# Kernel optimization log

Measured on AMD Instinct MI355X. Metric: run time of the kernel, lower is better.

## Reference

```python
import jax, jax.numpy as jnp
import numpy as np

EPS = 1e-5

def conv(x, w, groups=1):
    # x: NCHW, w: OIHW, VALID padding, stride 1 (cross-correlation, same as torch conv2d)
    return jax.lax.conv_general_dilated(x, w, (1, 1), 'VALID',
                                        feature_group_count=groups,
                                        dimension_numbers=('NCHW', 'OIHW', 'NCHW'))

def bn(x, g, b, m, v):
    # eval-mode batchnorm with running stats
    scale = (g / jnp.sqrt(v + EPS))[None, :, None, None]
    return (x - m[None, :, None, None]) * scale + b[None, :, None, None]

def xcorr_depthwise(x, k):
    # x: [B,C,Hs,Ws] search, k: [B,C,Hk,Wk] per-sample kernels
    B, C, H, W = x.shape
    xr = x.reshape(1, B * C, H, W)
    kr = k.reshape(B * C, 1, k.shape[2], k.shape[3])
    out = conv(xr, kr, groups=B * C)  # [1, B*C, Ho, Wo]
    return out.reshape(B, C, out.shape[2], out.shape[3])

def setup_inputs() -> dict:
    key = jax.random.key(0)
    ks = jax.random.split(key, 16)
    Cin, Hid, Cout = 256, 256, 20
    inp = {
        'kernel': jax.random.normal(ks[0], (128, Cin, 7, 7), jnp.float32),
        'search': jax.random.normal(ks[1], (128, Cin, 31, 31), jnp.float32),
        'wk': jax.random.normal(ks[2], (Hid, Cin, 3, 3), jnp.float32) * 0.02,
        'gk': jnp.ones((Hid,), jnp.float32),
        'bk': jnp.zeros((Hid,), jnp.float32),
        'mk': jax.random.normal(ks[3], (Hid,), jnp.float32) * 0.1,
        'vk': jax.random.uniform(ks[4], (Hid,), jnp.float32) + 0.5,
        'ws': jax.random.normal(ks[5], (Hid, Cin, 3, 3), jnp.float32) * 0.02,
        'gs': jnp.ones((Hid,), jnp.float32),
        'bs': jnp.zeros((Hid,), jnp.float32),
        'ms': jax.random.normal(ks[6], (Hid,), jnp.float32) * 0.1,
        'vs': jax.random.uniform(ks[7], (Hid,), jnp.float32) + 0.5,
        'wh1': jax.random.normal(ks[8], (Hid, Hid, 1, 1), jnp.float32) * 0.02,
        'gh': jnp.ones((Hid,), jnp.float32),
        'bh': jnp.zeros((Hid,), jnp.float32),
        'mh': jax.random.normal(ks[9], (Hid,), jnp.float32) * 0.1,
        'vh': jax.random.uniform(ks[10], (Hid,), jnp.float32) + 0.5,
        'wh2': jax.random.normal(ks[11], (Cout, Hid, 1, 1), jnp.float32) * 0.02,
        'bh2': jnp.zeros((Cout,), jnp.float32),
    }
    return inp

def reference(kernel, search, wk, gk, bk, mk, vk, ws, gs, bs, ms, vs,
              wh1, gh, bh, mh, vh, wh2, bh2):
    k = jax.nn.relu(bn(conv(kernel, wk), gk, bk, mk, vk))   # [B,256,5,5]
    s = jax.nn.relu(bn(conv(search, ws), gs, bs, ms, vs))   # [B,256,29,29]
    f = xcorr_depthwise(s, k)                               # [B,256,25,25]
    h = jax.nn.relu(bn(conv(f, wh1), gh, bh, mh, vh))
    out = conv(h, wh2) + bh2[None, :, None, None]           # [B,20,25,25]
    return out
```

## Files before the change

### kernel.cpp

```cpp
#include <hip/hip_runtime.h>

typedef __bf16 bf16x8 __attribute__((ext_vector_type(8)));
typedef float floatx4 __attribute__((ext_vector_type(4)));
typedef unsigned short u16;
typedef unsigned int u32;

__device__ __forceinline__ u16 f2bf(float f) {
    union { float f; unsigned int u; } q; q.f = f;
    unsigned int r = q.u + 0x7FFFu + ((q.u >> 16) & 1u);
    return (u16)(r >> 16);
}
__device__ __forceinline__ float bf2f(u16 b) {
    union { unsigned int u; float f; } q; q.u = ((unsigned int)b) << 16;
    return q.f;
}

__device__ __forceinline__ void gl2lds16(const u16* g, u16* l) {
    __builtin_amdgcn_global_load_lds((const __attribute__((address_space(1))) u32*)g,
                                     (__attribute__((address_space(3))) u32*)l, 16, 0, 0);
}

__global__ __launch_bounds__(256) void prep_all(
    const float* __restrict__ wk, const float* __restrict__ wsw, const float* __restrict__ wh1,
    const float* __restrict__ gk, const float* __restrict__ bk,
    const float* __restrict__ mk, const float* __restrict__ vk,
    const float* __restrict__ gs, const float* __restrict__ bs,
    const float* __restrict__ ms, const float* __restrict__ vs,
    const float* __restrict__ gh, const float* __restrict__ bh,
    const float* __restrict__ mh, const float* __restrict__ vh,
    u16* __restrict__ WKP, u16* __restrict__ WSP, u16* __restrict__ WH1P,
    float* __restrict__ par)
{
    int bid = blockIdx.x, t = threadIdx.x;
    if (bid < 4608) {
        const float* src = (bid < 2304) ? wk : wsw;
        u16* dst = (bid < 2304) ? WKP : WSP;
        int tid = ((bid < 2304) ? bid : bid - 2304) * 256 + t;
        int o  = tid / 2304;
        int k  = tid - o * 2304;
        int rc = k >> 8;
        int ci = k & 255;
        dst[tid] = f2bf(src[o * 2304 + ci * 9 + rc]);
    } else if (bid < 4864) {
        int tid = (bid - 4608) * 256 + t;
        WH1P[tid] = f2bf(wh1[tid]);
    } else {
        float s;
        s = gk[t] * rsqrtf(vk[t] + 1e-5f); par[0*256+t] = s; par[1*256+t] = bk[t] - mk[t]*s;
        s = gs[t] * rsqrtf(vs[t] + 1e-5f); par[2*256+t] = s; par[3*256+t] = bs[t] - ms[t]*s;
        s = gh[t] * rsqrtf(vh[t] + 1e-5f); par[4*256+t] = s; par[5*256+t] = bh[t] - mh[t]*s;
    }
}

__global__ __launch_bounds__(256) void nchw2nhwc_both(
    const float* __restrict__ kin, u16* __restrict__ KIN,
    const float* __restrict__ sin_, u16* __restrict__ SIN)
{
    __shared__ float tile[64][33];
    int bid = blockIdx.x;
    const float* in; u16* out; int HW, sptiles;
    if (bid < 1024) { in = kin;  out = KIN; HW = 49;  sptiles = 2; }
    else { bid -= 1024; in = sin_; out = SIN; HW = 961; sptiles = 31; }
    int st  = bid % sptiles;
    int tmp = bid / sptiles;
    int ct  = tmp & 3;
    int b   = tmp >> 2;
    int sp0 = st * 32, ci0 = ct * 64;
    int t = threadIdx.x;
    int j = t & 31, i8 = t >> 5;
    const float* ip = in + ((size_t)b * 256 + ci0 + i8) * HW + sp0 + j;
#pragma unroll
    for (int k = 0; k < 8; ++k) {
        if (sp0 + j < HW) tile[i8 + k * 8][j] = ip[(size_t)(k * 8) * HW];
    }
    __syncthreads();
    int cl = t & 63, s4 = t >> 6;
#pragma unroll
    for (int k = 0; k < 8; ++k) {
        int spl = s4 + k * 4;
        int sp  = sp0 + spl;
        if (sp < HW) out[((size_t)b * HW + sp) * 256 + ci0 + cl] = f2bf(tile[cl][spl]);
    }
}

__global__ __launch_bounds__(256) void conv_gemm(
    const u16* __restrict__ Ain, const u16* __restrict__ Wpk,
    const float* __restrict__ scale, const float* __restrict__ shift,
    u16* __restrict__ Out,
    int OHW, int OW, int IW, int bstride, int KW, int nrc, int mblocks)
{
    __shared__ u16 Alds[4096];
    __shared__ u16 Blds[4096];

    const int tot = mblocks * 2;
    const int grp = (tot >> 3) << 3;
    const int lid = blockIdx.x;
    const int nid = (lid < grp) ? ((lid & 7) * (grp >> 3) + (lid >> 3)) : lid;
    const int m0 = (nid >> 1) * 128;
    const int n0 = (nid & 1) * 128;

    const int t    = threadIdx.x;
    const int wave = t >> 6;
    const int lane = t & 63;
    const int quad = lane >> 4;
    const int lrow = lane & 15;

    const int koff = (((t & 3) ^ ((t >> 3) & 3)) << 3);
    const int r0 = t >> 2;
    int m_a0 = m0 + r0;
    int b0 = m_a0 / OHW; int rem0 = m_a0 - b0 * OHW; int y0 = rem0 / OW; int x0 = rem0 - y0 * OW;
    int m_a1 = m_a0 + 64;
    int b1 = m_a1 / OHW; int rem1 = m_a1 - b1 * OHW; int y1 = rem1 / OW; int x1 = rem1 - y1 * OW;
    const u16* ag0 = Ain + (size_t)b0 * bstride + (size_t)(y0 * IW + x0) * 256 + koff;
    const u16* ag1 = Ain + (size_t)b1 * bstride + (size_t)(y1 * IW + x1) * 256 + koff;
    const int Ktot = nrc * 256;
    const u16* bg0 = Wpk + (size_t)(n0 + r0) * Ktot + koff;
    const u16* bg1 = bg0 + (size_t)64 * Ktot;

    u16* lA0 = Alds + wave * 512;
    u16* lA1 = Alds + 2048 + wave * 512;
    u16* lB0 = Blds + wave * 512;
    u16* lB1 = Blds + 2048 + wave * 512;

    floatx4 zero = {0.f, 0.f, 0.f, 0.f};
    floatx4 acc[4][4];
#pragma unroll
    for (int i = 0; i < 4; ++i)
#pragma unroll
        for (int j = 0; j < 4; ++j) acc[i][j] = zero;

    const int wr  = (wave >> 1) << 6;
    const int wc  = (wave & 1) << 6;
    const int pos = ((quad ^ ((lrow >> 1) & 3)) << 3);

    const int nchunks = nrc << 3;
    for (int ch = 0; ch < nchunks; ++ch) {
        int rc  = ch >> 3;
        int ci0 = (ch & 7) << 5;
        int rr  = rc / KW;
        int cc  = rc - rr * KW;
        int ao  = (rr * IW + cc) * 256 + ci0;
        int bo  = ch << 5;
        __syncthreads();
        gl2lds16(ag0 + ao, lA0);
        gl2lds16(ag1 + ao, lA1);
        gl2lds16(bg0 + bo, lB0);
        gl2lds16(bg1 + bo, lB1);
        __syncthreads();
        bf16x8 af[4], bfr[4];
#pragma unroll
        for (int mi = 0; mi < 4; ++mi)
            af[mi] = *(const bf16x8*)&Alds[(wr + mi * 16 + lrow) * 32 + pos];
#pragma unroll
        for (int ni = 0; ni < 4; ++ni)
            bfr[ni] = *(const bf16x8*)&Blds[(wc + ni * 16 + lrow) * 32 + pos];
#pragma unroll
        for (int mi = 0; mi < 4; ++mi)
#pragma unroll
            for (int ni = 0; ni < 4; ++ni)
                acc[mi][ni] = __builtin_amdgcn_mfma_f32_16x16x32_bf16(af[mi], bfr[ni], acc[mi][ni], 0, 0, 0);
    }

    float sc[4], sh[4];
#pragma unroll
    for (int ni = 0; ni < 4; ++ni) {
        int gn = n0 + wc + ni * 16 + lrow;
        sc[ni] = scale[gn];
        sh[ni] = shift[gn];
    }
#pragma unroll
    for (int mi = 0; mi < 4; ++mi) {
        int gm = m0 + wr + mi * 16 + (quad << 2);
#pragma unroll
        for (int ri = 0; ri < 4; ++ri) {
            size_t ro = (size_t)(gm + ri) * 256 + n0 + wc + lrow;
#pragma unroll
            for (int ni = 0; ni < 4; ++ni) {
                float v = acc[mi][ni][ri] * sc[ni] + sh[ni];
                v = fmaxf(v, 0.f);
                Out[ro + ni * 16] = f2bf(v);
            }
        }
    }
}

#define NS_BLK 421
__global__ __launch_bounds__(512, 2) void conv_gemm256(
    const u16* __restrict__ AinS, const u16* __restrict__ WpkS,
    const float* __restrict__ parS, u16* __restrict__ OutS,
    const u16* __restrict__ AinK, const u16* __restrict__ WpkK,
    const float* __restrict__ parK, u16* __restrict__ OutK)
{
    __shared__ __align__(16) u16 Alds[2][256][64];
    __shared__ __align__(16) u16 Blds[2][256][64];

    const int Ktot = 2304;
    const int NKT  = 36;
    const int KW   = 3;

    const int lid = blockIdx.x;
    const bool isk = (lid >= NS_BLK);

    int nid;
    if (!isk) {
        const int xcd = lid & 7, sub = lid >> 3;
        nid = (xcd < 5) ? (xcd * 53 + sub) : (265 + (xcd - 5) * 52 + sub);
    } else {
        nid = lid - NS_BLK;
    }
    const int m0 = nid << 8;

    const int OHW     = isk ? 25    : 841;
    const int OW      = isk ? 5     : 29;
    const int IW      = isk ? 7     : 31;
    const int bstride = isk ? 12544 : 246016;
    const int Mtot    = isk ? 3200  : 107648;
    const u16* Ain    = isk ? AinK : AinS;
    const u16* Wpk    = isk ? WpkK : WpkS;
    const float* scale = isk ? parK : parS;
    const float* shift = scale + 256;
    u16* Out          = isk ? OutK : OutS;

    const int t     = threadIdx.x;
    const int wave  = t >> 6;
    const int lane  = t & 63;
    const int lrow  = lane & 15;
    const int lquad = lane >> 4;
    const int wmBase = (wave >> 2) << 7;
    const int wnBase = (wave & 3) << 6;

    const u16* pA[4];
    const u16* pB[4];
#pragma unroll
    for (int j = 0; j < 4; ++j) {
        int u = j * 512 + t;
        int row = u >> 3, slot = u & 7;
        int ko = ((slot ^ (row & 7)) << 3);
        int m = m0 + row; if (m >= Mtot) m = Mtot - 1;
        int b = m / OHW; int rem = m - b * OHW; int y = rem / OW; int x = rem - y * OW;
        pA[j] = Ain + (size_t)b * bstride + (size_t)(y * IW + x) * 256 + ko;
        pB[j] = Wpk + (size_t)row * (size_t)Ktot + ko;
    }

    const int xo0 = ((lquad ^ (lrow & 7)) << 3);
    const int xo1 = xo0 ^ 32;

    floatx4 acc[8][4];
#pragma unroll
    for (int i = 0; i < 8; ++i)
#pragma unroll
        for (int j = 0; j < 4; ++j) acc[i][j] = (floatx4){0.f, 0.f, 0.f, 0.f};

#pragma unroll
    for (int j = 0; j < 4; ++j)
        gl2lds16(pA[j], &Alds[0][0][0] + j * 4096 + wave * 512);
#pragma unroll
    for (int j = 0; j < 4; ++j)
        gl2lds16(pB[j], &Blds[0][0][0] + j * 4096 + wave * 512);
    asm volatile("s_waitcnt vmcnt(0)" ::: "memory");
    __builtin_amdgcn_s_barrier();

#define LOADA(mb) do {                                              \
        const u16* _p = Ab + (wmBase + (mb) * 16 + lrow) * 64;      \
        aF[0][0] = *(const bf16x8*)(_p + xo0);                      \
        aF[0][1] = *(const bf16x8*)(_p + xo1);                      \
        aF[1][0] = *(const bf16x8*)(_p + 1024 + xo0);               \
        aF[1][1] = *(const bf16x8*)(_p + 1024 + xo1);               \
    } while (0)

#define MFMA16(mb) do {                                                                               \
        _Pragma("unroll")                                                                             \
        for (int _n = 0; _n < 4; ++_n) {                                                              \
            acc[(mb)][_n]     = __builtin_amdgcn_mfma_f32_16x16x32_bf16(aF[0][0], bB[_n][0], acc[(mb)][_n], 0, 0, 0);     \
            acc[(mb)][_n]     = __builtin_amdgcn_mfma_f32_16x16x32_bf16(aF[0][1], bB[_n][1], acc[(mb)][_n], 0, 0, 0);     \
            acc[(mb) + 1][_n] = __builtin_amdgcn_mfma_f32_16x16x32_bf16(aF[1][0], bB[_n][0], acc[(mb) + 1][_n], 0, 0, 0); \
            acc[(mb) + 1][_n] = __builtin_amdgcn_mfma_f32_16x16x32_bf16(aF[1][1], bB[_n][1], acc[(mb) + 1][_n], 0, 0, 0); \
        }                                                                                             \
    } while (0)

#define PH_MID() do {                                        \
        __builtin_amdgcn_s_barrier();                        \
        asm volatile("s_waitcnt lgkmcnt(0)" ::: "memory");   \
        __builtin_amdgcn_s_setprio(1);                       \
    } while (0)

#define PH_END() do {                                        \
        __builtin_amdgcn_s_setprio(0);                       \
        __builtin_amdgcn_s_barrier();                        \
    } while (0)

#pragma unroll 2
    for (int kt = 0; kt < NKT; ++kt) {
        const int c = kt & 1;
        const u16* Ab = &Alds[c][0][0];
        const u16* Bb = &Blds[c][0][0];
        u16* An = &Alds[c ^ 1][0][0];
        u16* Bn = &Blds[c ^ 1][0][0];
        const int pf = (kt + 1 < NKT);
        const int kt1 = kt + 1;
        const int rc = kt1 >> 2;
        const int rr = rc / KW;
        const int cc = rc - rr * KW;
        const int aoffA = (rr * IW + cc) * 256 + ((kt1 & 3) << 6);
        const int boffB = kt1 << 6;

        bf16x8 bB[4][2];
        bf16x8 aF[2][2];

#pragma unroll
        for (int ni = 0; ni < 4; ++ni) {
            const u16* _p = Bb + (wnBase + ni * 16 + lrow) * 64;
            bB[ni][0] = *(const bf16x8*)(_p + xo0);
            bB[ni][1] = *(const bf16x8*)(_p + xo1);
        }
        LOADA(0);
        if (pf) {
#pragma unroll
            for (int j = 0; j < 4; ++j)
                gl2lds16(pA[j] + aoffA, An + j * 4096 + wave * 512);
        }
        PH_MID();
        MFMA16(0);
        PH_END();

        LOADA(2);
        if (pf) {
#pragma unroll
            for (int j = 0; j < 4; ++j)
                gl2lds16(pB[j] + boffB, Bn + j * 4096 + wave * 512);
        }
        PH_MID();
        MFMA16(2);
        PH_END();

        LOADA(4);
        PH_MID();
        MFMA16(4);
        PH_END();

        LOADA(6);
        PH_MID();
        MFMA16(6);
        __builtin_amdgcn_s_setprio(0);
        asm volatile("s_waitcnt vmcnt(0)" ::: "memory");
        __builtin_amdgcn_s_barrier();
    }

#undef LOADA
#undef MFMA16
#undef PH_MID
#undef PH_END

    float sc[4], sh[4];
#pragma unroll
    for (int ni = 0; ni < 4; ++ni) {
        int gn = wnBase + ni * 16 + lrow;
        sc[ni] = scale[gn];
        sh[ni] = shift[gn];
    }
#pragma unroll
    for (int mi = 0; mi < 8; ++mi) {
        int gm0 = m0 + wmBase + mi * 16 + (lquad << 2);
#pragma unroll
        for (int ri = 0; ri < 4; ++ri) {
            int gm = gm0 + ri;
            if (gm < Mtot) {
                size_t ro = (size_t)gm * 256 + wnBase + lrow;
#pragma unroll
                for (int ni = 0; ni < 4; ++ni) {
                    float v = acc[mi][ni][ri] * sc[ni] + sh[ni];
                    v = fmaxf(v, 0.f);
                    Out[ro + ni * 16] = f2bf(v);
                }
            }
        }
    }
}

__global__ __launch_bounds__(256) void xcorr(const u16* __restrict__ ss, const u16* __restrict__ kk,
                                             u16* __restrict__ f) {
    int lid = blockIdx.x;
    int bid = (lid & 7) * 400 + (lid >> 3);
    int b = bid / 25, y = bid - b * 25;
    int t = threadIdx.x;
    int cg = (t & 31) << 3;
    int xg = t >> 5;
    const u16* kbase = kk + (size_t)b * 25 * 256 + cg;
    const u16* sbase = ss + (size_t)(b * 29 + y) * 29 * 256 + cg;

    float acc[4][8];
#pragma unroll
    for (int j = 0; j < 4; ++j)
#pragma unroll
        for (int e = 0; e < 8; ++e) acc[j][e] = 0.f;

#pragma unroll
    for (int r = 0; r < 5; ++r) {
        const u16* srow = sbase + (size_t)r * 29 * 256;
#pragma unroll
        for (int c = 0; c < 5; ++c) {
            bf16x8 kv = *(const bf16x8*)(kbase + (r * 5 + c) * 256);
            float kf[8];
#pragma unroll
            for (int e = 0; e < 8; ++e) kf[e] = (float)kv[e];
#pragma unroll
            for (int j = 0; j < 4; ++j) {
                int x = xg + 8 * j;
                if (x < 25) {
                    bf16x8 sv = *(const bf16x8*)(srow + (size_t)(x + c) * 256);
#pragma unroll
                    for (int e = 0; e < 8; ++e) acc[j][e] += (float)sv[e] * kf[e];
                }
            }
        }
    }

    u16* fb = f + (size_t)(b * 25 + y) * 25 * 256 + cg;
#pragma unroll
    for (int j = 0; j < 4; ++j) {
        int x = xg + 8 * j;
        if (x < 25) {
            u16 pk[8];
#pragma unroll
            for (int e = 0; e < 8; ++e) pk[e] = f2bf(acc[j][e]);
            *(bf16x8*)(fb + (size_t)x * 256) = *(const bf16x8*)pk;
        }
    }
}

__global__ __launch_bounds__(256) void head(const u16* __restrict__ h, const float* __restrict__ w2,
                                            const float* __restrict__ b2, float* __restrict__ out) {
    __shared__ __align__(16) u16   hl[25 * 264];
    __shared__ __align__(16) float wl[20 * 260];
    int bid = blockIdx.x;
    int b = bid / 25, y = bid - b * 25;
    int t = threadIdx.x;
    const u16* hrow = h + (size_t)(b * 25 + y) * 25 * 256;
    for (int i = t; i < 800; i += 256) {
        int x = i >> 5, c8 = i & 31;
        *(bf16x8*)&hl[x * 264 + c8 * 8] = *(const bf16x8*)&hrow[i * 8];
    }
    for (int i = t; i < 1280; i += 256) {
        int co = i >> 6, c4 = i & 63;
        *(float4*)&wl[co * 260 + c4 * 4] = *(const float4*)&w2[(size_t)co * 256 + c4 * 4];
    }
    __syncthreads();
    for (int o = t; o < 500; o += 256) {
        int x = o / 20, co = o - x * 20;
        float acc = b2[co];
        const u16* hp = &hl[x * 264];
        const float* wp = &wl[co * 260];
#pragma unroll 4
        for (int k = 0; k < 256; k += 8) {
            bf16x8 hv = *(const bf16x8*)(hp + k);
            float4 w0 = *(const float4*)(wp + k);
            float4 w1v = *(const float4*)(wp + k + 4);
            acc += (float)hv[0] * w0.x + (float)hv[1] * w0.y
                 + (float)hv[2] * w0.z + (float)hv[3] * w0.w
                 + (float)hv[4] * w1v.x + (float)hv[5] * w1v.y
                 + (float)hv[6] * w1v.z + (float)hv[7] * w1v.w;
        }
        out[(size_t)((b * 20 + co) * 25 + y) * 25 + x] = acc;
    }
}

#define OFF_SIN  0ull
#define SZ_SIN   62980096ull
#define OFF_KIN  (OFF_SIN + SZ_SIN)
#define SZ_KIN   3211264ull
#define OFF_WKP  (OFF_KIN + SZ_KIN)
#define SZ_WKP   1179648ull
#define OFF_WSP  (OFF_WKP + SZ_WKP)
#define SZ_WSP   1179648ull
#define OFF_WH1P (OFF_WSP + SZ_WSP)
#define SZ_WH1P  131072ull
#define OFF_PAR  (OFF_WH1P + SZ_WH1P)
#define SZ_PAR   8192ull
#define OFF_KK   (OFF_PAR + SZ_PAR)
#define SZ_KK    1638400ull
#define OFF_SS   (OFF_KK + SZ_KK)
#define SZ_SS    55115776ull
#define OFF_F    OFF_SIN
#define OFF_H    OFF_SS

extern "C" void kernel_launch(void* const* d_in, const int* in_sizes, int n_in,
                              void* d_out, int out_size, void* d_ws, size_t ws_size,
                              hipStream_t stream) {
    const float* kin  = (const float*)d_in[0];
    const float* sin_ = (const float*)d_in[1];
    const float* wk   = (const float*)d_in[2];
    const float* gk   = (const float*)d_in[3];
    const float* bk   = (const float*)d_in[4];
    const float* mk   = (const float*)d_in[5];
    const float* vk   = (const float*)d_in[6];
    const float* wsw  = (const float*)d_in[7];
    const float* gs   = (const float*)d_in[8];
    const float* bs   = (const float*)d_in[9];
    const float* ms   = (const float*)d_in[10];
    const float* vs   = (const float*)d_in[11];
    const float* wh1  = (const float*)d_in[12];
    const float* gh   = (const float*)d_in[13];
    const float* bh   = (const float*)d_in[14];
    const float* mh   = (const float*)d_in[15];
    const float* vh   = (const float*)d_in[16];
    const float* wh2  = (const float*)d_in[17];
    const float* bh2  = (const float*)d_in[18];
    float* out = (float*)d_out;

    char* w = (char*)d_ws;
    u16*   SIN  = (u16*)(w + OFF_SIN);
    u16*   KIN  = (u16*)(w + OFF_KIN);
    u16*   WKP  = (u16*)(w + OFF_WKP);
    u16*   WSP  = (u16*)(w + OFF_WSP);
    u16*   WH1P = (u16*)(w + OFF_WH1P);
    float* PAR  = (float*)(w + OFF_PAR);
    u16*   KK   = (u16*)(w + OFF_KK);
    u16*   SS   = (u16*)(w + OFF_SS);
    u16*   F    = (u16*)(w + OFF_F);
    u16*   H    = (u16*)(w + OFF_H);

    prep_all<<<4865, 256, 0, stream>>>(wk, wsw, wh1,
                                       gk, bk, mk, vk, gs, bs, ms, vs, gh, bh, mh, vh,
                                       WKP, WSP, WH1P, PAR);
    nchw2nhwc_both<<<1024 + 15872, 256, 0, stream>>>(kin, KIN, sin_, SIN);

    conv_gemm256<<<434, 512, 0, stream>>>(SIN, WSP, PAR + 512, SS,
                                          KIN, WKP, PAR + 0, KK);
    xcorr<<<3200, 256, 0, stream>>>(SS, KK, F);
    conv_gemm<<<1250, 256, 0, stream>>>(F, WH1P, PAR + 1024, PAR + 1280, H,
                                        625, 25, 25, 160000, 1, 1, 625);
    head<<<3200, 256, 0, stream>>>(H, wh2, bh2, out);

    (void)in_sizes; (void)n_in; (void)out_size; (void)ws_size;
}
```

Before: 502.7 us.

## Merge prep and transpose kernels; simplify conv_gemm256 pipeline barriers

The weight/BN prep kernel and the NCHW-to-NHWC transpose kernel are merged into one launch, removing a kernel launch and the gap between the two. Inside the 256-thread GEMM main loop, the per-phase barriers and priority toggles are removed and all global-to-LDS prefetches for the next K tile are issued at the start of the iteration. This cuts barrier overhead but drops the interleaving of MFMA with loads and the wave-priority scheduling.

```diff
diff --git a/kernel.cpp b/kernel.cpp
--- a/kernel.cpp
+++ b/kernel.cpp
@@ -20,7 +20,9 @@
                                      (__attribute__((address_space(3))) u32*)l, 16, 0, 0);
 }
 
-__global__ __launch_bounds__(256) void prep_all(
+__global__ __launch_bounds__(256) void prep_and_transpose(
+    const float* __restrict__ kin, u16* __restrict__ KIN,
+    const float* __restrict__ sin_, u16* __restrict__ SIN,
     const float* __restrict__ wk, const float* __restrict__ wsw, const float* __restrict__ wh1,
     const float* __restrict__ gk, const float* __restrict__ bk,
     const float* __restrict__ mk, const float* __restrict__ vk,
@@ -31,7 +33,34 @@
     u16* __restrict__ WKP, u16* __restrict__ WSP, u16* __restrict__ WH1P,
     float* __restrict__ par)
 {
+    __shared__ float tile[64][33];
     int bid = blockIdx.x, t = threadIdx.x;
+    if (bid < 16896) {
+        const float* in; u16* out; int HW, sptiles;
+        if (bid < 1024) { in = kin;  out = KIN; HW = 49;  sptiles = 2; }
+        else { bid -= 1024; in = sin_; out = SIN; HW = 961; sptiles = 31; }
+        int st  = bid % sptiles;
+        int tmp = bid / sptiles;
+        int ct  = tmp & 3;
+        int b   = tmp >> 2;
+        int sp0 = st * 32, ci0 = ct * 64;
+        int j = t & 31, i8 = t >> 5;
+        const float* ip = in + ((size_t)b * 256 + ci0 + i8) * HW + sp0 + j;
+#pragma unroll
+        for (int k = 0; k < 8; ++k) {
+            if (sp0 + j < HW) tile[i8 + k * 8][j] = ip[(size_t)(k * 8) * HW];
+        }
+        __syncthreads();
+        int cl = t & 63, s4 = t >> 6;
+#pragma unroll
+        for (int k = 0; k < 8; ++k) {
+            int spl = s4 + k * 4;
+            int sp  = sp0 + spl;
+            if (sp < HW) out[((size_t)b * HW + sp) * 256 + ci0 + cl] = f2bf(tile[cl][spl]);
+        }
+        return;
+    }
+    bid -= 16896;
     if (bid < 4608) {
         const float* src = (bid < 2304) ? wk : wsw;
         u16* dst = (bid < 2304) ? WKP : WSP;
@@ -52,37 +81,6 @@
     }
 }
 
-__global__ __launch_bounds__(256) void nchw2nhwc_both(
-    const float* __restrict__ kin, u16* __restrict__ KIN,
-    const float* __restrict__ sin_, u16* __restrict__ SIN)
-{
-    __shared__ float tile[64][33];
-    int bid = blockIdx.x;
-    const float* in; u16* out; int HW, sptiles;
-    if (bid < 1024) { in = kin;  out = KIN; HW = 49;  sptiles = 2; }
-    else { bid -= 1024; in = sin_; out = SIN; HW = 961; sptiles = 31; }
-    int st  = bid % sptiles;
-    int tmp = bid / sptiles;
-    int ct  = tmp & 3;
-    int b   = tmp >> 2;
-    int sp0 = st * 32, ci0 = ct * 64;
-    int t = threadIdx.x;
-    int j = t & 31, i8 = t >> 5;
-    const float* ip = in + ((size_t)b * 256 + ci0 + i8) * HW + sp0 + j;
-#pragma unroll
-    for (int k = 0; k < 8; ++k) {
-        if (sp0 + j < HW) tile[i8 + k * 8][j] = ip[(size_t)(k * 8) * HW];
-    }
-    __syncthreads();
-    int cl = t & 63, s4 = t >> 6;
-#pragma unroll
-    for (int k = 0; k < 8; ++k) {
-        int spl = s4 + k * 4;
-        int sp  = sp0 + spl;
-        if (sp < HW) out[((size_t)b * HW + sp) * 256 + ci0 + cl] = f2bf(tile[cl][spl]);
-    }
-}
-
 __global__ __launch_bounds__(256) void conv_gemm(
     const u16* __restrict__ Ain, const u16* __restrict__ Wpk,
     const float* __restrict__ scale, const float* __restrict__ shift,
@@ -278,17 +276,6 @@
         }                                                                                             \
     } while (0)
 
-#define PH_MID() do {                                        \
-        __builtin_amdgcn_s_barrier();                        \
-        asm volatile("s_waitcnt lgkmcnt(0)" ::: "memory");   \
-        __builtin_amdgcn_s_setprio(1);                       \
-    } while (0)
-
-#define PH_END() do {                                        \
-        __builtin_amdgcn_s_setprio(0);                       \
-        __builtin_amdgcn_s_barrier();                        \
-    } while (0)
-
 #pragma unroll 2
     for (int kt = 0; kt < NKT; ++kt) {
         const int c = kt & 1;
@@ -304,9 +291,17 @@
         const int aoffA = (rr * IW + cc) * 256 + ((kt1 & 3) << 6);
         const int boffB = kt1 << 6;
 
+        if (pf) {
+#pragma unroll
+            for (int j = 0; j < 4; ++j)
+                gl2lds16(pA[j] + aoffA, An + j * 4096 + wave * 512);
+#pragma unroll
+            for (int j = 0; j < 4; ++j)
+                gl2lds16(pB[j] + boffB, Bn + j * 4096 + wave * 512);
+        }
+
         bf16x8 bB[4][2];
         bf16x8 aF[2][2];
-
 #pragma unroll
         for (int ni = 0; ni < 4; ++ni) {
             const u16* _p = Bb + (wnBase + ni * 16 + lrow) * 64;
@@ -314,42 +309,20 @@
             bB[ni][1] = *(const bf16x8*)(_p + xo1);
         }
         LOADA(0);
-        if (pf) {
-#pragma unroll
-            for (int j = 0; j < 4; ++j)
-                gl2lds16(pA[j] + aoffA, An + j * 4096 + wave * 512);
-        }
-        PH_MID();
         MFMA16(0);
-        PH_END();
-
         LOADA(2);
-        if (pf) {
-#pragma unroll
-            for (int j = 0; j < 4; ++j)
-                gl2lds16(pB[j] + boffB, Bn + j * 4096 + wave * 512);
-        }
-        PH_MID();
         MFMA16(2);
-        PH_END();
-
         LOADA(4);
-        PH_MID();
         MFMA16(4);
-        PH_END();
-
         LOADA(6);
-        PH_MID();
         MFMA16(6);
-        __builtin_amdgcn_s_setprio(0);
+
         asm volatile("s_waitcnt vmcnt(0)" ::: "memory");
         __builtin_amdgcn_s_barrier();
     }
 
 #undef LOADA
 #undef MFMA16
-#undef PH_MID
-#undef PH_END
 
     float sc[4], sh[4];
 #pragma unroll
@@ -519,10 +492,10 @@
     u16*   F    = (u16*)(w + OFF_F);
     u16*   H    = (u16*)(w + OFF_H);
 
-    prep_all<<<4865, 256, 0, stream>>>(wk, wsw, wh1,
-                                       gk, bk, mk, vk, gs, bs, ms, vs, gh, bh, mh, vh,
-                                       WKP, WSP, WH1P, PAR);
-    nchw2nhwc_both<<<1024 + 15872, 256, 0, stream>>>(kin, KIN, sin_, SIN);
+    prep_and_transpose<<<21761, 256, 0, stream>>>(kin, KIN, sin_, SIN,
+                                                  wk, wsw, wh1,
+                                                  gk, bk, mk, vk, gs, bs, ms, vs, gh, bh, mh, vh,
+                                                  WKP, WSP, WH1P, PAR);
 
     conv_gemm256<<<434, 512, 0, stream>>>(SIN, WSP, PAR + 512, SS,
                                           KIN, WKP, PAR + 0, KK);
```

After: 484.9 us. -3.5%, faster.
